# Optimization experiments

Measured on AMD Instinct MI355X. Metric: run time of the kernel, lower is better.

Reference implementation:

```python
import jax, jax.numpy as jnp
import numpy as np

B, C_IN, L, NCLASS = 256, 6, 512, 10

def setup_inputs() -> dict:
    key = jax.random.key(0)
    ks = jax.random.split(key, 16)
    g = lambda k, shp, s=0.05: jax.random.normal(k, shp, dtype=jnp.float32) * s
    return {
        "x": jax.random.normal(ks[0], (B, C_IN, L), dtype=jnp.float32),
        "conv1_w": g(ks[1], (32, C_IN, 3)),
        "conv1_b": g(ks[2], (32,)),
        "bn1_g": jnp.ones((32,), jnp.float32),
        "bn1_b": jnp.zeros((32,), jnp.float32),
        "bn1_m": g(ks[3], (32,)),
        "bn1_v": jnp.abs(g(ks[4], (32,))) + 1.0,
        "conv2_w": g(ks[5], (64, 32, 3)),
        "conv2_b": g(ks[6], (64,)),
        "bn2_g": jnp.ones((64,), jnp.float32),
        "bn2_b": jnp.zeros((64,), jnp.float32),
        "bn2_m": g(ks[7], (64,)),
        "bn2_v": jnp.abs(g(ks[8], (64,))) + 1.0,
        "wq": g(ks[9], (64, 64)),
        "bq": g(ks[10], (64,)),
        "wk": g(ks[11], (64, 64)),
        "bk": g(ks[12], (64,)),
        "wv": g(ks[13], (64, 64)),
        "bv": g(ks[14], (64,)),
        "fc_w": g(ks[15], (NCLASS, 64)),
        "fc_b": jnp.zeros((NCLASS,), jnp.float32),
    }

def _conv1d(x, w, b):
    # x: [B, C, L], w: [O, C, 3], padding=1 -> same length
    y = jax.lax.conv_general_dilated(
        x, w, window_strides=(1,), padding=[(1, 1)],
        dimension_numbers=("NCH", "OIH", "NCH"))
    return y + b[None, :, None]

def _bn(x, g, b, m, v, eps=1e-5):
    # eval-mode BatchNorm1d over channel dim of [B, C, L]
    inv = g * jax.lax.rsqrt(v + eps)
    return x * inv[None, :, None] + (b - m * inv)[None, :, None]

def reference(x, conv1_w, conv1_b, bn1_g, bn1_b, bn1_m, bn1_v,
              conv2_w, conv2_b, bn2_g, bn2_b, bn2_m, bn2_v,
              wq, bq, wk, bk, wv, bv, fc_w, fc_b):
    h = jax.nn.relu(_bn(_conv1d(x, conv1_w, conv1_b), bn1_g, bn1_b, bn1_m, bn1_v))
    h = jax.nn.relu(_bn(_conv1d(h, conv2_w, conv2_b), bn2_g, bn2_b, bn2_m, bn2_v))
    h = h.transpose(0, 2, 1)                      # [B, L, 64]
    q = h @ wq.T + bq
    k = h @ wk.T + bk
    v = h @ wv.T + bv
    scores = jnp.einsum("bqd,bkd->bqk", q, k) / jnp.sqrt(jnp.float32(64.0))
    attn = jax.nn.softmax(scores, axis=-1)
    out = jnp.einsum("bqk,bkd->bqd", attn, v)     # [B, L, 64]
    pooled = out.mean(axis=1)                     # [B, 64]
    return pooled @ fc_w.T + fc_b                 # [B, n_class]
```

## Files before the change

kernel.cpp:

```cpp
#include <hip/hip_runtime.h>
#include <hip/hip_bf16.h>


#define NB 256
#define LL 512
#define CIN 6
#define NCLASS 10
#define SLAB 9472
#define QSC 0.18033688f

typedef __bf16 bf16x8 __attribute__((ext_vector_type(8)));
typedef float f32x4 __attribute__((ext_vector_type(4)));
typedef unsigned short us4 __attribute__((ext_vector_type(4)));

static __device__ __forceinline__ unsigned short f2b(float f) {
    __bf16 h = (__bf16)f;
    return __builtin_bit_cast(unsigned short, h);
}

__global__ __launch_bounds__(256) void prep_weights(
    const float* __restrict__ w1, const float* __restrict__ cb1,
    const float* __restrict__ g1, const float* __restrict__ be1,
    const float* __restrict__ m1, const float* __restrict__ v1,
    const float* __restrict__ w2, const float* __restrict__ cb2,
    const float* __restrict__ g2, const float* __restrict__ be2,
    const float* __restrict__ m2, const float* __restrict__ v2,
    const float* __restrict__ wq, const float* __restrict__ wk,
    const float* __restrict__ wv,
    unsigned short* __restrict__ w1p, float* __restrict__ b1f,
    unsigned short* __restrict__ w2p, float* __restrict__ b2f,
    unsigned short* __restrict__ wqp, unsigned short* __restrict__ wkp,
    unsigned short* __restrict__ wvp)
{
    const int t = threadIdx.x;
    for (int idx = t; idx < 1024; idx += 256) {
        int c = idx >> 5, k = idx & 31;
        int dl = k >> 3, ci = k & 7;
        float inv = g1[c] * rsqrtf(v1[c] + 1e-5f);
        float val = (dl < 3 && ci < 6) ? w1[c * 18 + ci * 3 + dl] * inv : 0.f;
        w1p[idx] = f2b(val);
    }
    if (t < 32) {
        float inv = g1[t] * rsqrtf(v1[t] + 1e-5f);
        b1f[t] = be1[t] + (cb1[t] - m1[t]) * inv;
    }
    for (int idx = t; idx < 2048; idx += 256) {
        int c2 = idx >> 5, ci = idx & 31;
        float inv = g2[c2] * rsqrtf(v2[c2] + 1e-5f);
        const float* wp = w2 + c2 * 96 + ci * 3;
        w2p[c2 * 96 +      ci] = f2b(wp[0] * inv);
        w2p[c2 * 96 + 32 + ci] = f2b(wp[1] * inv);
        w2p[c2 * 96 + 64 + ci] = f2b(wp[2] * inv);
    }
    if (t >= 64 && t < 128) {
        int c2 = t - 64;
        float inv = g2[c2] * rsqrtf(v2[c2] + 1e-5f);
        b2f[c2] = be2[c2] + (cb2[c2] - m2[c2]) * inv;
    }
    for (int idx = t; idx < 4096; idx += 256) {
        wqp[idx] = f2b(wq[idx] * QSC);
        wkp[idx] = f2b(wk[idx]);
        wvp[idx] = f2b(wv[idx]);
    }
}

__global__ __launch_bounds__(1024, 4) void fused_all(
    const float* __restrict__ x,
    const unsigned short* __restrict__ w1p, const float* __restrict__ b1f,
    const unsigned short* __restrict__ w2p, const float* __restrict__ b2f,
    const unsigned short* __restrict__ wqp, const unsigned short* __restrict__ wkp,
    const unsigned short* __restrict__ wvp,
    const float* __restrict__ bq, const float* __restrict__ bk,
    const float* __restrict__ bvp,
    const float* __restrict__ fcw, const float* __restrict__ fcb,
    float* __restrict__ outp)
{
    const int b = blockIdx.x;
    const int t = threadIdx.x;
    const int w = t >> 6, lane = t & 63, quad = lane >> 4, lc = lane & 15;

    __shared__ __align__(16) char smem[16 * SLAB + 6144];
    char* myslab = smem + w * SLAB;
    unsigned short* h1sl = (unsigned short*)(myslab + 3072);
    unsigned short* Ts   = (unsigned short*)(myslab + 4608);
    unsigned short* Kf   = (unsigned short*)myslab;
    unsigned short* Vf   = (unsigned short*)(myslab + 4096);
    unsigned short* Ps   = (unsigned short*)(myslab + 8192);
    float* redw   = (float*)(myslab + 8192);
    float* pooled = (float*)(smem + 8448);
    unsigned short* xstage = (unsigned short*)(smem + 16 * SLAB);

    if (t < 768) {
        int ci = t >> 7, j4 = (t & 127) * 4;
        float4 xv = *(const float4*)(x + ((size_t)b * CIN + ci) * LL + j4);
        us4 pk;
        pk[0] = f2b(xv.x); pk[1] = f2b(xv.y); pk[2] = f2b(xv.z); pk[3] = f2b(xv.w);
        *(us4*)&xstage[ci * 512 + j4] = pk;
    }
    __syncthreads();

    bf16x8 bW1[2];
    #pragma unroll
    for (int nt = 0; nt < 2; nt++)
        bW1[nt] = *(const bf16x8*)(w1p + (nt * 16 + lc) * 32 + quad * 8);
    float b1v[2] = {b1f[lc], b1f[16 + lc]};
    f32x4 h1acc[3][2];
    #pragma unroll
    for (int mt = 0; mt < 3; mt++) {
        int pos = w * 32 - 2 + mt * 16 + lc + quad;
        bool ok = (quad < 3) && (pos >= 0) && (pos < LL);
        int posc = pos < 0 ? 0 : (pos > 511 ? 511 : pos);
        bf16x8 aX;
        #pragma unroll
        for (int u = 0; u < 6; u++) {
            __bf16 vb = __builtin_bit_cast(__bf16, xstage[u * 512 + posc]);
            aX[u] = ok ? vb : (__bf16)0.f;
        }
        aX[6] = (__bf16)0.f; aX[7] = (__bf16)0.f;
        #pragma unroll
        for (int nt = 0; nt < 2; nt++) {
            f32x4 z = {0.f, 0.f, 0.f, 0.f};
            h1acc[mt][nt] = __builtin_amdgcn_mfma_f32_16x16x32_bf16(aX, bW1[nt], z, 0, 0, 0);
        }
    }
    #pragma unroll
    for (int mt = 0; mt < 3; mt++)
        #pragma unroll
        for (int nt = 0; nt < 2; nt++)
            #pragma unroll
            for (int r = 0; r < 4; r++) {
                int j = mt * 16 + quad * 4 + r;
                if (j < 34) {
                    int pos = w * 32 - 1 + j;
                    float y = h1acc[mt][nt][r] + b1v[nt];
                    y = (pos >= 0 && pos < LL && y > 0.f) ? y : 0.f;
                    h1sl[j * 40 + nt * 16 + lc] = f2b(y);
                }
            }

    bf16x8 bX[2][3], aW2[4][3];
    #pragma unroll
    for (int rt = 0; rt < 2; rt++)
        #pragma unroll
        for (int kc = 0; kc < 3; kc++)
            bX[rt][kc] = *(const bf16x8*)&h1sl[(rt * 16 + lc + kc) * 40 + quad * 8];
    #pragma unroll
    for (int nt = 0; nt < 4; nt++)
        #pragma unroll
        for (int kc = 0; kc < 3; kc++)
            aW2[nt][kc] = *(const bf16x8*)(w2p + (nt * 16 + lc) * 96 + kc * 32 + quad * 8);

    f32x4 acc2[4][2];
    #pragma unroll
    for (int nt = 0; nt < 4; nt++)
        #pragma unroll
        for (int rt = 0; rt < 2; rt++) {
            f32x4 a = {0.f, 0.f, 0.f, 0.f};
            a = __builtin_amdgcn_mfma_f32_16x16x32_bf16(aW2[nt][0], bX[rt][0], a, 0, 0, 0);
            a = __builtin_amdgcn_mfma_f32_16x16x32_bf16(aW2[nt][1], bX[rt][1], a, 0, 0, 0);
            acc2[nt][rt] = __builtin_amdgcn_mfma_f32_16x16x32_bf16(aW2[nt][2], bX[rt][2], a, 0, 0, 0);
        }

    #pragma unroll
    for (int nt = 0; nt < 4; nt++) {
        const float4 bb2 = *(const float4*)&b2f[nt * 16 + quad * 4];
        #pragma unroll
        for (int rt = 0; rt < 2; rt++) {
            us4 pk;
            float y0 = acc2[nt][rt][0] + bb2.x; pk[0] = f2b(y0 > 0.f ? y0 : 0.f);
            float y1 = acc2[nt][rt][1] + bb2.y; pk[1] = f2b(y1 > 0.f ? y1 : 0.f);
            float y2 = acc2[nt][rt][2] + bb2.z; pk[2] = f2b(y2 > 0.f ? y2 : 0.f);
            float y3 = acc2[nt][rt][3] + bb2.w; pk[3] = f2b(y3 > 0.f ? y3 : 0.f);
            *(us4*)&Ts[(rt * 16 + lc) * 72 + nt * 16 + quad * 4] = pk;
        }
    }
    bf16x8 aH[2][2];
    #pragma unroll
    for (int rt = 0; rt < 2; rt++)
        #pragma unroll
        for (int kc = 0; kc < 2; kc++)
            aH[rt][kc] = *(const bf16x8*)&Ts[(rt * 16 + lc) * 72 + kc * 32 + quad * 8];

    bf16x8 aQ[2][2];
    for (int p = 0; p < 2; p++) {
        const unsigned short* wsrc = p ? wkp : wqp;
        const float* bsrc = p ? bk : bq;
        const float bscl = p ? 1.0f : QSC;
        #pragma unroll
        for (int nt = 0; nt < 4; nt++) {
            bf16x8 aW[2];
            #pragma unroll
            for (int kc = 0; kc < 2; kc++)
                aW[kc] = *(const bf16x8*)(wsrc + (nt * 16 + lc) * 64 + kc * 32 + quad * 8);
            float4 bb = *(const float4*)&bsrc[nt * 16 + quad * 4];
            bb.x *= bscl; bb.y *= bscl; bb.z *= bscl; bb.w *= bscl;
            #pragma unroll
            for (int rt = 0; rt < 2; rt++) {
                f32x4 a = {0.f, 0.f, 0.f, 0.f};
                a = __builtin_amdgcn_mfma_f32_16x16x32_bf16(aW[0], aH[rt][0], a, 0, 0, 0);
                a = __builtin_amdgcn_mfma_f32_16x16x32_bf16(aW[1], aH[rt][1], a, 0, 0, 0);
                us4 pk;
                pk[0] = f2b(a[0] + bb.x); pk[1] = f2b(a[1] + bb.y);
                pk[2] = f2b(a[2] + bb.z); pk[3] = f2b(a[3] + bb.w);
                *(us4*)&Ts[(rt * 16 + lc) * 72 + nt * 16 + quad * 4] = pk;
            }
        }
        #pragma unroll
        for (int rt = 0; rt < 2; rt++)
            #pragma unroll
            for (int kc = 0; kc < 2; kc++) {
                bf16x8 fr = *(const bf16x8*)&Ts[(rt * 16 + lc) * 72 + kc * 32 + quad * 8];
                if (p == 0) aQ[rt][kc] = fr;
                else *(bf16x8*)&Kf[((rt * 2 + kc) << 9) + lane * 8] = fr;
            }
    }

    #pragma unroll
    for (int nt = 0; nt < 4; nt++) {
        bf16x8 bW[2];
        #pragma unroll
        for (int kc = 0; kc < 2; kc++)
            bW[kc] = *(const bf16x8*)(wvp + (nt * 16 + lc) * 64 + kc * 32 + quad * 8);
        const float bvv = bvp[nt * 16 + lc];
        #pragma unroll
        for (int rt = 0; rt < 2; rt++) {
            f32x4 a = {0.f, 0.f, 0.f, 0.f};
            a = __builtin_amdgcn_mfma_f32_16x16x32_bf16(aH[rt][0], bW[0], a, 0, 0, 0);
            a = __builtin_amdgcn_mfma_f32_16x16x32_bf16(aH[rt][1], bW[1], a, 0, 0, 0);
            #pragma unroll
            for (int reg = 0; reg < 4; reg++)
                Vf[nt * 512 + (quad * 16 + lc) * 8 + reg * 2 + rt] = f2b(a[reg] + bvv);
        }
    }

    __syncthreads();

    f32x4 outacc[2][4];
    #pragma unroll
    for (int rt = 0; rt < 2; rt++)
        #pragma unroll
        for (int dt = 0; dt < 4; dt++) outacc[rt][dt] = (f32x4){0.f, 0.f, 0.f, 0.f};
    float den[2][4] = {{0.f, 0.f, 0.f, 0.f}, {0.f, 0.f, 0.f, 0.f}};

    bf16x8 bK[2][2], bKn[2][2];
    {
        const unsigned short* sK = (const unsigned short*)smem;
        #pragma unroll
        for (int nt = 0; nt < 2; nt++)
            #pragma unroll
            for (int kc = 0; kc < 2; kc++)
                bK[nt][kc] = *(const bf16x8*)&sK[((nt * 2 + kc) << 9) + lane * 8];
    }

    for (int cc = 0; cc < 16; cc++) {
        f32x4 sv[2][2];
        #pragma unroll
        for (int rt = 0; rt < 2; rt++)
            #pragma unroll
            for (int nt = 0; nt < 2; nt++) {
                f32x4 z = {0.f, 0.f, 0.f, 0.f};
                z = __builtin_amdgcn_mfma_f32_16x16x32_bf16(aQ[rt][0], bK[nt][0], z, 0, 0, 0);
                sv[rt][nt] = __builtin_amdgcn_mfma_f32_16x16x32_bf16(aQ[rt][1], bK[nt][1], z, 0, 0, 0);
            }
        const unsigned short* sV = (const unsigned short*)(smem + cc * SLAB + 4096);
        bf16x8 bV[4];
        #pragma unroll
        for (int dt = 0; dt < 4; dt++)
            bV[dt] = *(const bf16x8*)&sV[dt * 512 + lane * 8];
        #pragma unroll
        for (int reg = 0; reg < 4; reg++) {
            float p0 = __builtin_amdgcn_exp2f(sv[0][0][reg]);
            float p1 = __builtin_amdgcn_exp2f(sv[0][1][reg]);
            den[0][reg] += p0 + p1;
            unsigned pk32 = (unsigned)f2b(p0) | ((unsigned)f2b(p1) << 16);
            *(unsigned*)&Ps[(quad * 4 + reg) * 40 + lc * 2] = pk32;
        }
        if (cc < 15) {
            const unsigned short* sKn = (const unsigned short*)(smem + (cc + 1) * SLAB);
            #pragma unroll
            for (int nt = 0; nt < 2; nt++)
                #pragma unroll
                for (int kc = 0; kc < 2; kc++)
                    bKn[nt][kc] = *(const bf16x8*)&sKn[((nt * 2 + kc) << 9) + lane * 8];
        }
        bf16x8 aP0 = *(const bf16x8*)&Ps[lc * 40 + quad * 8];
        #pragma unroll
        for (int reg = 0; reg < 4; reg++) {
            float p0 = __builtin_amdgcn_exp2f(sv[1][0][reg]);
            float p1 = __builtin_amdgcn_exp2f(sv[1][1][reg]);
            den[1][reg] += p0 + p1;
            unsigned pk32 = (unsigned)f2b(p0) | ((unsigned)f2b(p1) << 16);
            *(unsigned*)&Ps[(quad * 4 + reg) * 40 + lc * 2] = pk32;
        }
        #pragma unroll
        for (int dt = 0; dt < 4; dt++)
            outacc[0][dt] = __builtin_amdgcn_mfma_f32_16x16x32_bf16(aP0, bV[dt], outacc[0][dt], 0, 0, 0);
        bf16x8 aP1 = *(const bf16x8*)&Ps[lc * 40 + quad * 8];
        #pragma unroll
        for (int dt = 0; dt < 4; dt++)
            outacc[1][dt] = __builtin_amdgcn_mfma_f32_16x16x32_bf16(aP1, bV[dt], outacc[1][dt], 0, 0, 0);
        #pragma unroll
        for (int nt = 0; nt < 2; nt++)
            #pragma unroll
            for (int kc = 0; kc < 2; kc++)
                bK[nt][kc] = bKn[nt][kc];
    }

    float rden[2][4];
    #pragma unroll
    for (int rt = 0; rt < 2; rt++)
        #pragma unroll
        for (int reg = 0; reg < 4; reg++) {
            float d2 = den[rt][reg];
            d2 += __shfl_xor(d2, 1);  d2 += __shfl_xor(d2, 2);
            d2 += __shfl_xor(d2, 4);  d2 += __shfl_xor(d2, 8);
            rden[rt][reg] = 1.0f / d2;
        }
    #pragma unroll
    for (int dt = 0; dt < 4; dt++) {
        float ps = 0.f;
        #pragma unroll
        for (int rt = 0; rt < 2; rt++)
            #pragma unroll
            for (int reg = 0; reg < 4; reg++)
                ps += outacc[rt][dt][reg] * rden[rt][reg];
        ps += __shfl_xor(ps, 16);
        ps += __shfl_xor(ps, 32);
        if (quad == 0) redw[dt * 16 + lc] = ps;
    }
    __syncthreads();
    if (t < 64) {
        float s = 0.f;
        #pragma unroll
        for (int ww = 0; ww < 16; ww++)
            s += *(const float*)(smem + ww * SLAB + 8192 + t * 4);
        pooled[t] = s * (1.0f / 512.0f);
    }
    __syncthreads();
    if (t < NCLASS) {
        float acc = fcb[t];
        #pragma unroll
        for (int d = 0; d < 64; d++) acc += pooled[d] * fcw[t * 64 + d];
        outp[b * NCLASS + t] = acc;
    }
}

extern "C" void kernel_launch(void* const* d_in, const int* in_sizes, int n_in,
                              void* d_out, int out_size, void* d_ws, size_t ws_size,
                              hipStream_t stream)
{
    const float* x   = (const float*)d_in[0];
    const float* w1  = (const float*)d_in[1];
    const float* cb1 = (const float*)d_in[2];
    const float* g1  = (const float*)d_in[3];
    const float* be1 = (const float*)d_in[4];
    const float* m1  = (const float*)d_in[5];
    const float* v1  = (const float*)d_in[6];
    const float* w2  = (const float*)d_in[7];
    const float* cb2 = (const float*)d_in[8];
    const float* g2  = (const float*)d_in[9];
    const float* be2 = (const float*)d_in[10];
    const float* m2  = (const float*)d_in[11];
    const float* v2  = (const float*)d_in[12];
    const float* wq  = (const float*)d_in[13];
    const float* bq  = (const float*)d_in[14];
    const float* wk  = (const float*)d_in[15];
    const float* bk  = (const float*)d_in[16];
    const float* wv  = (const float*)d_in[17];
    const float* bv  = (const float*)d_in[18];
    const float* fcw = (const float*)d_in[19];
    const float* fcb = (const float*)d_in[20];
    float* out = (float*)d_out;

    char* ws = (char*)d_ws;
    unsigned short* w1p = (unsigned short*)(ws);
    float*          b1f = (float*)(ws + 2048u);
    float*          b2f = (float*)(ws + 2176u);
    unsigned short* w2p = (unsigned short*)(ws + 2432u);
    unsigned short* wqp = (unsigned short*)(ws + 14720u);
    unsigned short* wkp = (unsigned short*)(ws + 22912u);
    unsigned short* wvp = (unsigned short*)(ws + 31104u);

    prep_weights<<<dim3(1), 256, 0, stream>>>(w1, cb1, g1, be1, m1, v1,
                                              w2, cb2, g2, be2, m2, v2,
                                              wq, wk, wv,
                                              w1p, b1f, w2p, b2f, wqp, wkp, wvp);
    fused_all<<<dim3(NB), 1024, 0, stream>>>(x, w1p, b1f, w2p, b2f,
                                             wqp, wkp, wvp,
                                             bq, bk, bv, fcw, fcb, out);
}
```

Before: 136.4 us.

## Compute transposed scores so softmax probabilities feed PV MFMA from registers

Swaps the MFMA operand order in the QK^T product so each lane holds score values already in the A-operand layout needed for the P·V MFMA. This removes the LDS round trip (write P, read back as bf16x8) and its associated latency per key chunk. The V tile layout is changed to match, with a vectorized us4 store. The denominator reduction becomes a cross-quad shuffle plus a broadcast shuffle. It risks subtle layout mismatches, but the loads and stores are kept consistent.

```diff
diff --git a/kernel.cpp b/kernel.cpp
--- a/kernel.cpp
+++ b/kernel.cpp
@@ -85,7 +85,6 @@
     unsigned short* Ts   = (unsigned short*)(myslab + 4608);
     unsigned short* Kf   = (unsigned short*)myslab;
     unsigned short* Vf   = (unsigned short*)(myslab + 4096);
-    unsigned short* Ps   = (unsigned short*)(myslab + 8192);
     float* redw   = (float*)(myslab + 8192);
     float* pooled = (float*)(smem + 8448);
     unsigned short* xstage = (unsigned short*)(smem + 16 * SLAB);
@@ -227,9 +226,10 @@
             f32x4 a = {0.f, 0.f, 0.f, 0.f};
             a = __builtin_amdgcn_mfma_f32_16x16x32_bf16(aH[rt][0], bW[0], a, 0, 0, 0);
             a = __builtin_amdgcn_mfma_f32_16x16x32_bf16(aH[rt][1], bW[1], a, 0, 0, 0);
-            #pragma unroll
-            for (int reg = 0; reg < 4; reg++)
-                Vf[nt * 512 + (quad * 16 + lc) * 8 + reg * 2 + rt] = f2b(a[reg] + bvv);
+            us4 pk;
+            pk[0] = f2b(a[0] + bvv); pk[1] = f2b(a[1] + bvv);
+            pk[2] = f2b(a[2] + bvv); pk[3] = f2b(a[3] + bvv);
+            *(us4*)&Vf[nt * 512 + quad * 128 + lc * 8 + rt * 4] = pk;
         }
     }
 
@@ -240,7 +240,7 @@
     for (int rt = 0; rt < 2; rt++)
         #pragma unroll
         for (int dt = 0; dt < 4; dt++) outacc[rt][dt] = (f32x4){0.f, 0.f, 0.f, 0.f};
-    float den[2][4] = {{0.f, 0.f, 0.f, 0.f}, {0.f, 0.f, 0.f, 0.f}};
+    float den[2] = {0.f, 0.f};
 
     bf16x8 bK[2][2], bKn[2][2];
     {
@@ -255,26 +255,18 @@
     for (int cc = 0; cc < 16; cc++) {
         f32x4 sv[2][2];
         #pragma unroll
-        for (int rt = 0; rt < 2; rt++)
-            #pragma unroll
-            for (int nt = 0; nt < 2; nt++) {
+        for (int nt = 0; nt < 2; nt++)
+            #pragma unroll
+            for (int rt = 0; rt < 2; rt++) {
                 f32x4 z = {0.f, 0.f, 0.f, 0.f};
-                z = __builtin_amdgcn_mfma_f32_16x16x32_bf16(aQ[rt][0], bK[nt][0], z, 0, 0, 0);
-                sv[rt][nt] = __builtin_amdgcn_mfma_f32_16x16x32_bf16(aQ[rt][1], bK[nt][1], z, 0, 0, 0);
+                z = __builtin_amdgcn_mfma_f32_16x16x32_bf16(bK[nt][0], aQ[rt][0], z, 0, 0, 0);
+                sv[nt][rt] = __builtin_amdgcn_mfma_f32_16x16x32_bf16(bK[nt][1], aQ[rt][1], z, 0, 0, 0);
             }
         const unsigned short* sV = (const unsigned short*)(smem + cc * SLAB + 4096);
         bf16x8 bV[4];
         #pragma unroll
         for (int dt = 0; dt < 4; dt++)
             bV[dt] = *(const bf16x8*)&sV[dt * 512 + lane * 8];
-        #pragma unroll
-        for (int reg = 0; reg < 4; reg++) {
-            float p0 = __builtin_amdgcn_exp2f(sv[0][0][reg]);
-            float p1 = __builtin_amdgcn_exp2f(sv[0][1][reg]);
-            den[0][reg] += p0 + p1;
-            unsigned pk32 = (unsigned)f2b(p0) | ((unsigned)f2b(p1) << 16);
-            *(unsigned*)&Ps[(quad * 4 + reg) * 40 + lc * 2] = pk32;
-        }
         if (cc < 15) {
             const unsigned short* sKn = (const unsigned short*)(smem + (cc + 1) * SLAB);
             #pragma unroll
@@ -283,22 +275,22 @@
                 for (int kc = 0; kc < 2; kc++)
                     bKn[nt][kc] = *(const bf16x8*)&sKn[((nt * 2 + kc) << 9) + lane * 8];
         }
-        bf16x8 aP0 = *(const bf16x8*)&Ps[lc * 40 + quad * 8];
-        #pragma unroll
-        for (int reg = 0; reg < 4; reg++) {
-            float p0 = __builtin_amdgcn_exp2f(sv[1][0][reg]);
-            float p1 = __builtin_amdgcn_exp2f(sv[1][1][reg]);
-            den[1][reg] += p0 + p1;
-            unsigned pk32 = (unsigned)f2b(p0) | ((unsigned)f2b(p1) << 16);
-            *(unsigned*)&Ps[(quad * 4 + reg) * 40 + lc * 2] = pk32;
-        }
-        #pragma unroll
-        for (int dt = 0; dt < 4; dt++)
-            outacc[0][dt] = __builtin_amdgcn_mfma_f32_16x16x32_bf16(aP0, bV[dt], outacc[0][dt], 0, 0, 0);
-        bf16x8 aP1 = *(const bf16x8*)&Ps[lc * 40 + quad * 8];
-        #pragma unroll
-        for (int dt = 0; dt < 4; dt++)
-            outacc[1][dt] = __builtin_amdgcn_mfma_f32_16x16x32_bf16(aP1, bV[dt], outacc[1][dt], 0, 0, 0);
+        bf16x8 aP[2];
+        #pragma unroll
+        for (int rt = 0; rt < 2; rt++)
+            #pragma unroll
+            for (int nt = 0; nt < 2; nt++)
+                #pragma unroll
+                for (int reg = 0; reg < 4; reg++) {
+                    float p = __builtin_amdgcn_exp2f(sv[nt][rt][reg]);
+                    den[rt] += p;
+                    aP[rt][nt * 4 + reg] = (__bf16)p;
+                }
+        #pragma unroll
+        for (int dt = 0; dt < 4; dt++) {
+            outacc[0][dt] = __builtin_amdgcn_mfma_f32_16x16x32_bf16(aP[0], bV[dt], outacc[0][dt], 0, 0, 0);
+            outacc[1][dt] = __builtin_amdgcn_mfma_f32_16x16x32_bf16(aP[1], bV[dt], outacc[1][dt], 0, 0, 0);
+        }
         #pragma unroll
         for (int nt = 0; nt < 2; nt++)
             #pragma unroll
@@ -308,14 +300,15 @@
 
     float rden[2][4];
     #pragma unroll
-    for (int rt = 0; rt < 2; rt++)
-        #pragma unroll
-        for (int reg = 0; reg < 4; reg++) {
-            float d2 = den[rt][reg];
-            d2 += __shfl_xor(d2, 1);  d2 += __shfl_xor(d2, 2);
-            d2 += __shfl_xor(d2, 4);  d2 += __shfl_xor(d2, 8);
-            rden[rt][reg] = 1.0f / d2;
-        }
+    for (int rt = 0; rt < 2; rt++) {
+        float d2 = den[rt];
+        d2 += __shfl_xor(d2, 16);
+        d2 += __shfl_xor(d2, 32);
+        d2 = 1.0f / d2;
+        #pragma unroll
+        for (int reg = 0; reg < 4; reg++)
+            rden[rt][reg] = __shfl(d2, quad * 4 + reg);
+    }
     #pragma unroll
     for (int dt = 0; dt < 4; dt++) {
         float ps = 0.f;
```

Result: faster. 130.8 us (-4.1%).
